# Kernel optimization log

Measured on AMD Instinct MI355X. Metric: run time of the kernel, lower is better.

## Reference

```python
import jax, jax.numpy as jnp
import numpy as np

B, T, N, D = 32, 64, 300, 128


def setup_inputs() -> dict:
    key = jax.random.key(0)
    k1, k2, k3, k4 = jax.random.split(key, 4)
    src = jax.random.normal(k1, (B, T, N, D), dtype=jnp.float32)
    # Parameters are zeros-initialized in the original module (untrained);
    # use small random values so the reference computes nontrivial math.
    wt1 = jax.random.normal(k2, (D,), dtype=jnp.float32) * 0.1
    wt2 = jax.random.normal(k3, (N, D), dtype=jnp.float32) * 0.1
    wt3 = jax.random.normal(k4, (N,), dtype=jnp.float32) * 0.1
    return {"src": src, "wt1": wt1, "wt2": wt2, "wt3": wt3}


def reference(src, wt1, wt2, wt3):
    # src: [B, T, N, D]
    Q = jnp.einsum('btnd,d->btn', src, wt1)            # [B, T, N]
    K = jnp.einsum('n,btnd->btd', wt3, src)            # [B, T, D]
    # bilinear score: Q @ wt2 @ K^T per batch -> [B, T, T]
    scores = jnp.einsum('bqn,nd,bkd->bqk', Q, wt2, K)
    # NOTE: original applies softmax over dim=0 (the batch axis) — faithful here.
    att = jax.nn.softmax(scores, axis=0)               # [B, Tq, Tk]
    # time-mixing: 'btnd,bta->band' -> output indexed [b, a(=T), n, d]
    mixed = jnp.einsum('btnd,bta->band', src, att)     # [B, T, N, D]
    return src + mixed  # dropout = identity at eval
```

## Files before the change

### kernel.cpp

```cpp
#include <hip/hip_runtime.h>

#define Bb 32
#define Tt 64
#define Nn 300
#define Dd 128
#define NC (Nn * Dd)
#define BTND ((size_t)Tt * NC)

__global__ __launch_bounds__(256) void qk_kernel(
        const float* __restrict__ src, const float* __restrict__ wt1,
        const float* __restrict__ wt3, float* __restrict__ Q,
        float* __restrict__ K) {
    __shared__ float wt3_s[Nn];
    __shared__ float kred[4 * Dd];
    const int tid = threadIdx.x;
    const int wave = tid >> 6, lane = tid & 63;
    for (int i = tid; i < Nn; i += 256) wt3_s[i] = wt3[i];
    __syncthreads();
    const int d0 = lane * 2;
    const float2 w1 = *(const float2*)(wt1 + d0);
    const float* sbt = src + (size_t)blockIdx.x * NC;
    float* Qrow = Q + (size_t)blockIdx.x * Nn;
    float kx = 0.f, ky = 0.f;
    for (int n = wave; n < Nn; n += 4) {
        float2 v = *(const float2*)(sbt + n * Dd + d0);
        float q = v.x * w1.x + v.y * w1.y;
        #pragma unroll
        for (int off = 32; off > 0; off >>= 1) q += __shfl_down(q, off, 64);
        if (lane == 0) Qrow[n] = q;
        float w3 = wt3_s[n];
        kx = fmaf(w3, v.x, kx);
        ky = fmaf(w3, v.y, ky);
    }
    kred[wave * Dd + d0] = kx;
    kred[wave * Dd + d0 + 1] = ky;
    __syncthreads();
    if (tid < Dd) {
        float s = kred[tid] + kred[Dd + tid] + kred[2 * Dd + tid] + kred[3 * Dd + tid];
        K[(size_t)blockIdx.x * Dd + tid] = s;
    }
}

__global__ __launch_bounds__(128) void score_kernel(
        const float* __restrict__ Q, const float* __restrict__ K,
        const float* __restrict__ wt2, float* __restrict__ scores) {
    __shared__ float qs[Nn];
    __shared__ float qws[Dd];
    const int tid = threadIdx.x;
    const int bq = blockIdx.x;
    const float* Qrow = Q + (size_t)bq * Nn;
    for (int i = tid; i < Nn; i += 128) qs[i] = Qrow[i];
    __syncthreads();
    float qw = 0.f;
    for (int n = 0; n < Nn; ++n) qw = fmaf(qs[n], wt2[n * Dd + tid], qw);
    qws[tid] = qw;
    __syncthreads();
    if (tid < Tt) {
        const int b = bq >> 6;
        const float* Krow = K + (size_t)(b * Tt + tid) * Dd;
        float s = 0.f;
        for (int d = 0; d < Dd; ++d) s = fmaf(qws[d], Krow[d], s);
        scores[(size_t)bq * Tt + tid] = s;
    }
}

__global__ __launch_bounds__(256) void softmax_b_kernel(
        const float* __restrict__ scores, float* __restrict__ att) {
    const int idx = blockIdx.x * 256 + threadIdx.x;
    float v[Bb];
    float m = -1e30f;
    #pragma unroll
    for (int b = 0; b < Bb; ++b) {
        v[b] = scores[b * (Tt * Tt) + idx];
        m = fmaxf(m, v[b]);
    }
    float sum = 0.f;
    #pragma unroll
    for (int b = 0; b < Bb; ++b) {
        float e = __expf(v[b] - m);
        v[b] = e;
        sum += e;
    }
    const float inv = 1.0f / sum;
    #pragma unroll
    for (int b = 0; b < Bb; ++b) att[b * (Tt * Tt) + idx] = v[b] * inv;
}

__global__ __launch_bounds__(256, 4) void mix_kernel(
        const float* __restrict__ src, const float* __restrict__ att,
        float* __restrict__ out) {
    __shared__ float att_s[Tt * Tt];
    const int tid = threadIdx.x;
    const int b = blockIdx.y;
    for (int i = tid; i < Tt * Tt; i += 256) {
        int t = i >> 6, a = i & 63;
        float v = att[(size_t)b * Tt * Tt + i];
        att_s[i] = v + (t == a ? 1.0f : 0.0f);
    }
    __syncthreads();
    const int j = blockIdx.x * 256 + tid;
    const float* sb = src + (size_t)b * BTND + j;
    float* ob = out + (size_t)b * BTND + j;
    float acc[Tt];
    #pragma unroll
    for (int a = 0; a < Tt; ++a) acc[a] = 0.f;
    float x = sb[0];
    for (int t = 0; t < Tt; ++t) {
        float xn = 0.f;
        if (t < Tt - 1) xn = sb[(size_t)(t + 1) * NC];
        const float* arow = att_s + t * Tt;
        #pragma unroll
        for (int a = 0; a < Tt; ++a) acc[a] = fmaf(arow[a], x, acc[a]);
        x = xn;
    }
    #pragma unroll
    for (int a = 0; a < Tt; ++a) ob[(size_t)a * NC] = acc[a];
}

extern "C" void kernel_launch(void* const* d_in, const int* in_sizes, int n_in,
                              void* d_out, int out_size, void* d_ws, size_t ws_size,
                              hipStream_t stream) {
    const float* src = (const float*)d_in[0];
    const float* wt1 = (const float*)d_in[1];
    const float* wt2 = (const float*)d_in[2];
    const float* wt3 = (const float*)d_in[3];
    float* out = (float*)d_out;

    float* ws = (float*)d_ws;
    float* Q      = ws;
    float* K      = Q + (size_t)Bb * Tt * Nn;
    float* scores = K + (size_t)Bb * Tt * Dd;
    float* att    = scores + (size_t)Bb * Tt * Tt;

    qk_kernel<<<Bb * Tt, 256, 0, stream>>>(src, wt1, wt3, Q, K);
    score_kernel<<<Bb * Tt, 128, 0, stream>>>(Q, K, wt2, scores);
    softmax_b_kernel<<<(Tt * Tt) / 256, 256, 0, stream>>>(scores, att);
    dim3 g4(NC / 256, Bb);
    mix_kernel<<<g4, 256, 0, stream>>>(src, att, out);
}
```

Measured before the change: 750.3 us.

## Register-tile mix kernel over 8 output rows by 8 columns per thread

The time-mixing kernel now uses 512-thread blocks. Each wave owns 8 output time rows and each lane owns 8 contiguous feature columns, accumulating an 8x8 register tile. Attention rows are read from LDS as two float4 per step instead of 64 scalars, and src and out are accessed with float4. The aim is to cut LDS traffic per FMA and improve memory-access width. The cost is that every wave in a block reloads the same src columns, adding 8x redundant global/L2 reads.

```diff
diff --git a/kernel.cpp b/kernel.cpp
--- a/kernel.cpp
+++ b/kernel.cpp
@@ -86,35 +86,59 @@
     for (int b = 0; b < Bb; ++b) att[b * (Tt * Tt) + idx] = v[b] * inv;
 }
 
-__global__ __launch_bounds__(256, 4) void mix_kernel(
+#define MIX_JT 512
+__global__ __launch_bounds__(512, 2) void mix_kernel(
         const float* __restrict__ src, const float* __restrict__ att,
         float* __restrict__ out) {
     __shared__ float att_s[Tt * Tt];
     const int tid = threadIdx.x;
     const int b = blockIdx.y;
-    for (int i = tid; i < Tt * Tt; i += 256) {
+    for (int i = tid; i < Tt * Tt; i += 512) {
         int t = i >> 6, a = i & 63;
         float v = att[(size_t)b * Tt * Tt + i];
         att_s[i] = v + (t == a ? 1.0f : 0.0f);
     }
     __syncthreads();
-    const int j = blockIdx.x * 256 + tid;
+    const int wave = tid >> 6, lane = tid & 63;
+    const int a0 = wave * 8;
+    const int j = blockIdx.x * MIX_JT + lane * 8;
     const float* sb = src + (size_t)b * BTND + j;
     float* ob = out + (size_t)b * BTND + j;
-    float acc[Tt];
+    float acc[8][8];
     #pragma unroll
-    for (int a = 0; a < Tt; ++a) acc[a] = 0.f;
-    float x = sb[0];
+    for (int ai = 0; ai < 8; ++ai)
+        #pragma unroll
+        for (int jj = 0; jj < 8; ++jj) acc[ai][jj] = 0.f;
+    float4 x0 = *(const float4*)(sb);
+    float4 x1 = *(const float4*)(sb + 4);
     for (int t = 0; t < Tt; ++t) {
-        float xn = 0.f;
-        if (t < Tt - 1) xn = sb[(size_t)(t + 1) * NC];
-        const float* arow = att_s + t * Tt;
+        float4 n0 = x0, n1 = x1;
+        if (t < Tt - 1) {
+            n0 = *(const float4*)(sb + (size_t)(t + 1) * NC);
+            n1 = *(const float4*)(sb + (size_t)(t + 1) * NC + 4);
+        }
+        const float4 av0 = *(const float4*)(att_s + t * Tt + a0);
+        const float4 av1 = *(const float4*)(att_s + t * Tt + a0 + 4);
+        const float av[8] = {av0.x, av0.y, av0.z, av0.w,
+                             av1.x, av1.y, av1.z, av1.w};
+        const float xv[8] = {x0.x, x0.y, x0.z, x0.w,
+                             x1.x, x1.y, x1.z, x1.w};
         #pragma unroll
-        for (int a = 0; a < Tt; ++a) acc[a] = fmaf(arow[a], x, acc[a]);
-        x = xn;
+        for (int ai = 0; ai < 8; ++ai)
+            #pragma unroll
+            for (int jj = 0; jj < 8; ++jj)
+                acc[ai][jj] = fmaf(av[ai], xv[jj], acc[ai][jj]);
+        x0 = n0;
+        x1 = n1;
     }
     #pragma unroll
-    for (int a = 0; a < Tt; ++a) ob[(size_t)a * NC] = acc[a];
+    for (int ai = 0; ai < 8; ++ai) {
+        float* orow = ob + (size_t)(a0 + ai) * NC;
+        float4 s0 = {acc[ai][0], acc[ai][1], acc[ai][2], acc[ai][3]};
+        float4 s1 = {acc[ai][4], acc[ai][5], acc[ai][6], acc[ai][7]};
+        *(float4*)(orow) = s0;
+        *(float4*)(orow + 4) = s1;
+    }
 }
 
 extern "C" void kernel_launch(void* const* d_in, const int* in_sizes, int n_in,
@@ -135,6 +159,6 @@
     qk_kernel<<<Bb * Tt, 256, 0, stream>>>(src, wt1, wt3, Q, K);
     score_kernel<<<Bb * Tt, 128, 0, stream>>>(Q, K, wt2, scores);
     softmax_b_kernel<<<(Tt * Tt) / 256, 256, 0, stream>>>(scores, att);
-    dim3 g4(NC / 256, Bb);
-    mix_kernel<<<g4, 256, 0, stream>>>(src, att, out);
+    dim3 g4(NC / MIX_JT, Bb);
+    mix_kernel<<<g4, 512, 0, stream>>>(src, att, out);
 }
```

Result: no change. 761.8 us (+1.5%).

## Register-tile mix kernel with float4 columns and scalar attention loads

Applied to the files above, without the earlier changes.

Each wave in the mixing kernel now computes 16 output time steps for 4 contiguous columns using float4 loads/stores, reading attention weights as wave-uniform scalar loads instead of staging them in shared memory. The identity addition is folded into the softmax kernel. The Q/K projection kernel switches to 32-lane groups with float4 loads. The intent is to cut LDS traffic and widen memory accesses, at the cost of each src row being loaded by four waves.

```diff
diff --git a/kernel.cpp b/kernel.cpp
--- a/kernel.cpp
+++ b/kernel.cpp
@@ -12,31 +12,38 @@
         const float* __restrict__ wt3, float* __restrict__ Q,
         float* __restrict__ K) {
     __shared__ float wt3_s[Nn];
-    __shared__ float kred[4 * Dd];
+    __shared__ float kred[8 * Dd];
     const int tid = threadIdx.x;
-    const int wave = tid >> 6, lane = tid & 63;
+    const int grp = tid >> 5;
+    const int gl = tid & 31;
     for (int i = tid; i < Nn; i += 256) wt3_s[i] = wt3[i];
     __syncthreads();
-    const int d0 = lane * 2;
-    const float2 w1 = *(const float2*)(wt1 + d0);
+    const int d0 = gl * 4;
+    const float4 w1 = *(const float4*)(wt1 + d0);
     const float* sbt = src + (size_t)blockIdx.x * NC;
     float* Qrow = Q + (size_t)blockIdx.x * Nn;
-    float kx = 0.f, ky = 0.f;
-    for (int n = wave; n < Nn; n += 4) {
-        float2 v = *(const float2*)(sbt + n * Dd + d0);
-        float q = v.x * w1.x + v.y * w1.y;
-        #pragma unroll
-        for (int off = 32; off > 0; off >>= 1) q += __shfl_down(q, off, 64);
-        if (lane == 0) Qrow[n] = q;
-        float w3 = wt3_s[n];
-        kx = fmaf(w3, v.x, kx);
-        ky = fmaf(w3, v.y, ky);
+    float4 k = {0.f, 0.f, 0.f, 0.f};
+    for (int n0 = 0; n0 < Nn; n0 += 8) {
+        const int n = n0 + grp;
+        if (n < Nn) {
+            float4 v = *(const float4*)(sbt + n * Dd + d0);
+            float q = v.x * w1.x + v.y * w1.y + v.z * w1.z + v.w * w1.w;
+            #pragma unroll
+            for (int off = 16; off > 0; off >>= 1) q += __shfl_down(q, off, 32);
+            if (gl == 0) Qrow[n] = q;
+            const float w3 = wt3_s[n];
+            k.x = fmaf(w3, v.x, k.x);
+            k.y = fmaf(w3, v.y, k.y);
+            k.z = fmaf(w3, v.z, k.z);
+            k.w = fmaf(w3, v.w, k.w);
+        }
     }
-    kred[wave * Dd + d0] = kx;
-    kred[wave * Dd + d0 + 1] = ky;
+    *(float4*)(kred + grp * Dd + d0) = k;
     __syncthreads();
     if (tid < Dd) {
-        float s = kred[tid] + kred[Dd + tid] + kred[2 * Dd + tid] + kred[3 * Dd + tid];
+        float s = 0.f;
+        #pragma unroll
+        for (int g = 0; g < 8; ++g) s += kred[g * Dd + tid];
         K[(size_t)blockIdx.x * Dd + tid] = s;
     }
 }
@@ -82,39 +89,49 @@
         sum += e;
     }
     const float inv = 1.0f / sum;
+    const float diag = (idx % 65 == 0) ? 1.0f : 0.0f;
     #pragma unroll
-    for (int b = 0; b < Bb; ++b) att[b * (Tt * Tt) + idx] = v[b] * inv;
+    for (int b = 0; b < Bb; ++b) att[b * (Tt * Tt) + idx] = v[b] * inv + diag;
 }
 
+#define MIX_JT 256
 __global__ __launch_bounds__(256, 4) void mix_kernel(
-        const float* __restrict__ src, const float* __restrict__ att,
+        const float* __restrict__ src, const float* __restrict__ attI,
         float* __restrict__ out) {
-    __shared__ float att_s[Tt * Tt];
     const int tid = threadIdx.x;
     const int b = blockIdx.y;
-    for (int i = tid; i < Tt * Tt; i += 256) {
-        int t = i >> 6, a = i & 63;
-        float v = att[(size_t)b * Tt * Tt + i];
-        att_s[i] = v + (t == a ? 1.0f : 0.0f);
-    }
-    __syncthreads();
-    const int j = blockIdx.x * 256 + tid;
+    const int lane = tid & 63;
+    const int a0 = __builtin_amdgcn_readfirstlane((tid >> 6) * 16);
+    const int j = blockIdx.x * MIX_JT + lane * 4;
     const float* sb = src + (size_t)b * BTND + j;
     float* ob = out + (size_t)b * BTND + j;
-    float acc[Tt];
+    const float* ab = attI + ((size_t)b << 12) + a0;
+    float acc[16][4];
     #pragma unroll
-    for (int a = 0; a < Tt; ++a) acc[a] = 0.f;
-    float x = sb[0];
+    for (int ai = 0; ai < 16; ++ai)
+        #pragma unroll
+        for (int jj = 0; jj < 4; ++jj) acc[ai][jj] = 0.f;
+    float4 x = *(const float4*)sb;
     for (int t = 0; t < Tt; ++t) {
-        float xn = 0.f;
-        if (t < Tt - 1) xn = sb[(size_t)(t + 1) * NC];
-        const float* arow = att_s + t * Tt;
+        const int tn = (t < Tt - 1) ? t + 1 : t;
+        const float4 xn = *(const float4*)(sb + (size_t)tn * NC);
+        float av[16];
         #pragma unroll
-        for (int a = 0; a < Tt; ++a) acc[a] = fmaf(arow[a], x, acc[a]);
+        for (int i = 0; i < 16; ++i) av[i] = ab[t * Tt + i];
+        #pragma unroll
+        for (int ai = 0; ai < 16; ++ai) {
+            acc[ai][0] = fmaf(av[ai], x.x, acc[ai][0]);
+            acc[ai][1] = fmaf(av[ai], x.y, acc[ai][1]);
+            acc[ai][2] = fmaf(av[ai], x.z, acc[ai][2]);
+            acc[ai][3] = fmaf(av[ai], x.w, acc[ai][3]);
+        }
         x = xn;
     }
     #pragma unroll
-    for (int a = 0; a < Tt; ++a) ob[(size_t)a * NC] = acc[a];
+    for (int ai = 0; ai < 16; ++ai) {
+        float4 s = {acc[ai][0], acc[ai][1], acc[ai][2], acc[ai][3]};
+        *(float4*)(ob + (size_t)(a0 + ai) * NC) = s;
+    }
 }
 
 extern "C" void kernel_launch(void* const* d_in, const int* in_sizes, int n_in,
@@ -135,6 +152,6 @@
     qk_kernel<<<Bb * Tt, 256, 0, stream>>>(src, wt1, wt3, Q, K);
     score_kernel<<<Bb * Tt, 128, 0, stream>>>(Q, K, wt2, scores);
     softmax_b_kernel<<<(Tt * Tt) / 256, 256, 0, stream>>>(scores, att);
-    dim3 g4(NC / 256, Bb);
+    dim3 g4(NC / MIX_JT, Bb);
     mix_kernel<<<g4, 256, 0, stream>>>(src, att, out);
 }
```

New measurement: 820.1 us. 9.3% more time.
